# Kernel optimization log

Hardware: AMD Instinct MI355X
Metric: run time of the kernel (lower is better)

The kernel has to match this reference:

```python
import jax, jax.numpy as jnp
import numpy as np

N_NODES = 50000
N_EDGES = 800000
NIN = 128
NHID = 128
NLAYERS = 4
NOUT = 40
H = 0.1
EPS_BN = 1e-5
CG_ITERS = 10


def _bn(x, g, b, m, v):
    # eval-mode BatchNorm1d with running stats
    return (x - m) * jax.lax.rsqrt(v + EPS_BN) * g + b


def _forward(T, edge_index, Kopen_W, Kopen_b, bnO_g, bnO_b, bnO_m, bnO_v, conv_W, conv_b, bnA_g, bnA_b, bnA_m, bnA_v, Wq, bq, Wk, bk, mha_factor, KR1_W, KR1_b, KR2_W, KR2_b, KRU0_W, KRU0_b, bn_g, bn_b, bn_m, bn_v, Kappa, Kclose_W, Kclose_b):
    N = T.shape[0]
    L = KR1_W.shape[0]
    order = L
    row, col = edge_index[0], edge_index[1]
    # get_laplacian(sym) removes self-loops, so L = I - D^{-1/2} A D^{-1/2} on non-loop edges
    nonself = (row != col).astype(jnp.float32)
    deg = jax.ops.segment_sum(nonself, row, num_segments=N)
    dinv = jnp.where(deg > 0, jax.lax.rsqrt(jnp.maximum(deg, 1.0)), 0.0)
    lap_w = -(dinv[row] * dinv[col]) * nonself  # off-diagonal Laplacian weights; diagonal = 1

    Th = jax.nn.elu(_bn(T @ Kopen_W.T + Kopen_b, bnO_g, bnO_b, bnO_m, bnO_v))
    T0 = Th  # dropout is identity in eval mode
    # Conv1d(k=1) over `order` identical repeated history slots == one dense matmul
    z = jax.nn.relu(_bn(T0 @ conv_W.T + conv_b, bnA_g, bnA_b, bnA_m, bnA_v))
    acts = jnp.tile(z[None], (order, 1, 1))  # [order, N, nhid]
    nhid = Th.shape[1]
    scale = nhid ** -0.5  # single head -> head_dim = nhid
    rfac = jax.nn.relu(mha_factor[0])

    Tcur = Th
    for jj in range(L):
        # single-head self-attention weights over history axis (batch = nodes); output proj unused
        q = jnp.einsum('onh,dh->ond', acts, Wq) + bq
        k = jnp.einsum('onh,dh->ond', acts, Wk) + bk
        attn = jax.nn.softmax(jnp.einsum('ind,jnd->nij', q, k) * scale, axis=-1)  # [N, order, order]
        Cm = jnp.mean(jnp.log(attn * rfac + 1e-4), axis=0)
        Cm = 0.5 * (Cm + Cm.T)
        c = Cm[-1]
        c = c / jnp.sum(c)
        T1 = jnp.einsum('o,onh->nh', c, acts)
        # gated reaction MLP
        dT = T1 @ KR1_W[jj].T + KR1_b[jj] + T0 @ KRU0_W[jj].T + KRU0_b[jj]
        dT2 = T1 @ KR2_W[jj].T + KR2_b[jj]
        dT = dT + T1 * jnp.clip(dT2, -1.0, 1.0)
        Tr = jax.nn.elu(_bn(T1 + H * dT, bn_g[jj], bn_b[jj], bn_m[jj], bn_v[jj]))
        # implicit diffusion: CG iterations on (I + h*Kd*L) X = Tr
        Kd = jnp.clip(Kappa[jj], 0.0, 1.0)

        def matvec(Y):
            lapY = Y + jax.ops.segment_sum(lap_w[:, None] * Y[col], row, num_segments=N)
            return Y + H * (lapY * Kd)

        X, R, P = Tr, Tr, Tr
        normRold = jnp.sum(R * R)
        done = jnp.asarray(False)
        for _ in range(CG_ITERS):
            LP = matvec(P)
            alpha = jnp.sum(R * R) / (jnp.sum(P * LP) + 1e-6)
            Xn = X + alpha * P
            Rn = R - alpha * LP
            normR = jnp.sum(Rn * Rn)
            beta = normR / (normRold + 1e-6)
            Pn = Rn + beta * P
            X = jnp.where(done, X, Xn)
            R = jnp.where(done, R, Rn)
            done2 = done | (normR < 1e-5)  # early-break in torch -> freeze state
            P = jnp.where(done2, P, Pn)
            normRold = jnp.where(done2, normRold, normR)
            done = done2
        Tcur = X
        acts = jnp.concatenate([acts[1:], Tcur[None]], axis=0)
    return Tcur @ Kclose_W.T + Kclose_b


def setup_inputs():
    key = jax.random.key(0)
    ks = iter(jax.random.split(key, 64))
    f32 = jnp.float32

    def nrm(shape, s=0.05):
        return s * jax.random.normal(next(ks), shape, dtype=f32)

    def bn_params(shape):
        g = 1.0 + nrm(shape, 0.1)
        b = nrm(shape, 0.1)
        m = nrm(shape, 0.1)
        v = 1.0 + 0.1 * jax.random.uniform(next(ks), shape, dtype=f32)
        return g, b, m, v

    eye = jnp.eye(NHID, dtype=f32)
    d = {}
    d['T'] = jax.random.normal(next(ks), (N_NODES, NIN), dtype=f32)
    d['edge_index'] = jax.random.randint(next(ks), (2, N_EDGES), 0, N_NODES)
    d['Kopen_W'] = nrm((NHID, NIN), 0.08)
    d['Kopen_b'] = jnp.zeros((NHID,), f32)
    d['bnO_g'], d['bnO_b'], d['bnO_m'], d['bnO_v'] = bn_params((NHID,))
    d['conv_W'] = nrm((NHID, NHID), 0.08)
    d['conv_b'] = jnp.zeros((NHID,), f32)
    d['bnA_g'], d['bnA_b'], d['bnA_m'], d['bnA_v'] = bn_params((NHID,))
    d['Wq'] = nrm((NHID, NHID), 0.08)
    d['bq'] = jnp.zeros((NHID,), f32)
    d['Wk'] = nrm((NHID, NHID), 0.08)
    d['bk'] = jnp.zeros((NHID,), f32)
    d['mha_factor'] = jnp.array([10.0], dtype=f32)
    d['KR1_W'] = eye[None] + nrm((NLAYERS, NHID, NHID), 0.01)
    d['KR1_b'] = jnp.zeros((NLAYERS, NHID), f32)
    d['KR2_W'] = nrm((NLAYERS, NHID, NHID), 0.01)
    d['KR2_b'] = jnp.zeros((NLAYERS, NHID), f32)
    d['KRU0_W'] = eye[None] + nrm((NLAYERS, NHID, NHID), 0.01)
    d['KRU0_b'] = jnp.zeros((NLAYERS, NHID), f32)
    d['bn_g'], d['bn_b'], d['bn_m'], d['bn_v'] = bn_params((NLAYERS, NHID))
    d['Kappa'] = jax.random.uniform(next(ks), (NLAYERS, NHID), dtype=f32, minval=0.0, maxval=1.2)
    d['Kclose_W'] = nrm((NOUT, NHID), 0.08)
    d['Kclose_b'] = jnp.zeros((NOUT,), f32)
    return d


def reference(T, edge_index, Kopen_W, Kopen_b, bnO_g, bnO_b, bnO_m, bnO_v, conv_W, conv_b, bnA_g, bnA_b, bnA_m, bnA_v, Wq, bq, Wk, bk, mha_factor, KR1_W, KR1_b, KR2_W, KR2_b, KRU0_W, KRU0_b, bn_g, bn_b, bn_m, bn_v, Kappa, Kclose_W, Kclose_b):
    return _forward(T, edge_index, Kopen_W, Kopen_b, bnO_g, bnO_b, bnO_m, bnO_v, conv_W, conv_b, bnA_g, bnA_b, bnA_m, bnA_v, Wq, bq, Wk, bk, mha_factor, KR1_W, KR1_b, KR2_W, KR2_b, KRU0_W, KRU0_b, bn_g, bn_b, bn_m, bn_v, Kappa, Kclose_W, Kclose_b)
```

## Files before the change

kernel.cpp:

```cpp
#include <hip/hip_runtime.h>
#include <math.h>

#define N_NODES 50000
#define N_EDGES 800000
#define NHID    128
#define NOUT    40
#define NLAYERS 4
#define CG_ITERS 10
#define HSTEP   0.1f
#define EPS_BN  1e-5f

#define NB   (N_NODES * NHID)
#define NB4  (NB / 4)

#define EW_BLOCKS   2048
#define SPMV_BLOCKS 2048
#define ATTN_BLOCKS 1024
#define SCAN_BLOCKS 196

#define SLOT_RR   0
#define SLOT_PLP  10
#define SLOT_NR   20

__device__ __forceinline__ float wred64(float v) {
    v += __shfl_xor(v, 32, 64);
    v += __shfl_xor(v, 16, 64);
    v += __shfl_xor(v, 8, 64);
    v += __shfl_xor(v, 4, 64);
    v += __shfl_xor(v, 2, 64);
    v += __shfl_xor(v, 1, 64);
    return v;
}

__device__ __forceinline__ int wscan64(int v, int lane) {
    int incl = v;
    #pragma unroll
    for (int off = 1; off < 64; off <<= 1) {
        int t = __shfl_up(incl, off, 64);
        if (lane >= off) incl += t;
    }
    return incl;
}


__global__ void k_zero_i32(int* p, int n) {
    int i = blockIdx.x * blockDim.x + threadIdx.x;
    int stride = gridDim.x * blockDim.x;
    for (; i < n; i += stride) p[i] = 0;
}

__global__ void k_count(const int* __restrict__ row, const int* __restrict__ col, int* __restrict__ deg) {
    int e = blockIdx.x * 256 + threadIdx.x;
    if (e < N_EDGES) {
        int r = row[e], c = col[e];
        if (r != c) atomicAdd(&deg[r], 1);
    }
}

__global__ __launch_bounds__(256) void k_scan1(const int* __restrict__ deg,
                                               int* __restrict__ rowptr, int* __restrict__ blksum) {
    __shared__ int wsum[4];
    int tid = threadIdx.x, lane = tid & 63, wid = tid >> 6;
    int i = blockIdx.x * 256 + tid;
    int v = (i < N_NODES) ? deg[i] : 0;
    int incl = wscan64(v, lane);
    if (lane == 63) wsum[wid] = incl;
    __syncthreads();
    int wpre = 0;
    for (int w = 0; w < wid; w++) wpre += wsum[w];
    incl += wpre;
    if (i < N_NODES) rowptr[i + 1] = incl;
    if (tid == 255) blksum[blockIdx.x] = incl;
}

__global__ __launch_bounds__(256) void k_scan2(const int* __restrict__ blksum, int* __restrict__ blkoff) {
    __shared__ int wsum[4];
    int tid = threadIdx.x, lane = tid & 63, wid = tid >> 6;
    int v = (tid < SCAN_BLOCKS) ? blksum[tid] : 0;
    int incl = wscan64(v, lane);
    if (lane == 63) wsum[wid] = incl;
    __syncthreads();
    int wpre = 0;
    for (int w = 0; w < wid; w++) wpre += wsum[w];
    incl += wpre;
    if (tid < SCAN_BLOCKS) blkoff[tid] = incl - v;
}

__global__ __launch_bounds__(256) void k_scan3(const int* __restrict__ deg, const int* __restrict__ blkoff,
                                               int* __restrict__ rowptr, float* __restrict__ dinv,
                                               int* __restrict__ cursor) {
    int i = blockIdx.x * 256 + threadIdx.x;
    if (i == 0) rowptr[0] = 0;
    if (i < N_NODES) {
        int incl = rowptr[i + 1] + blkoff[blockIdx.x];
        rowptr[i + 1] = incl;
        int d = deg[i];
        cursor[i] = incl - d;
        dinv[i] = (d > 0) ? rsqrtf((float)d) : 0.0f;
    }
}

__global__ void k_scatter(const int* __restrict__ row, const int* __restrict__ col,
                          const float* __restrict__ dinv, int* __restrict__ cursor,
                          int* __restrict__ ecol, float* __restrict__ ew) {
    int e = blockIdx.x * 256 + threadIdx.x;
    if (e < N_EDGES) {
        int r = row[e], c = col[e];
        if (r != c) {
            int p = atomicAdd(&cursor[r], 1);
            ecol[p] = c;
            ew[p] = -dinv[r] * dinv[c];
        }
    }
}


__global__ void k_mmat(const float* __restrict__ Wq, const float* __restrict__ Wk, float* __restrict__ M) {
    int h1 = blockIdx.x, h2 = threadIdx.x;
    float s = 0.f;
    for (int d = 0; d < 128; ++d) s += Wq[d * 128 + h1] * Wk[d * 128 + h2];
    M[h1 * 128 + h2] = s;
}

__global__ void k_uv(const float* __restrict__ Wq, const float* __restrict__ Wk,
// ... 121 lines not shown
    int tid = threadIdx.x;
    int lane = tid & 63, wid = tid >> 6;
    const float* hp[4] = {h0, h1, h2, h3};
    const float* gp[4] = {g0, g1, g2, g3};
    float uu0 = u[lane], uu1 = u[lane + 64];
    float vv0 = v[lane], vv1 = v[lane + 64];
    float c0v = *c0p;
    float rf = mha[0]; rf = rf > 0.f ? rf : 0.f;
    const float scale = 0.08838834764831845f;

    float tacc = 0.f;
    int totalWaves = gridDim.x * 4;
    for (int n = blockIdx.x * 4 + wid; n < N_NODES; n += totalWaves) {
        float a0[4], a1[4], gg0[4], gg1[4];
        size_t base = (size_t)n * 128 + lane;
        #pragma unroll
        for (int o = 0; o < 4; o++) {
            a0[o] = hp[o][base];  a1[o] = hp[o][base + 64];
            gg0[o] = gp[o][base]; gg1[o] = gp[o][base + 64];
        }
        float s[4][4], pu[4], pv[4];
        #pragma unroll
        for (int i = 0; i < 4; i++) {
            pu[i] = wred64(uu0 * a0[i] + uu1 * a1[i]);
            pv[i] = wred64(vv0 * a0[i] + vv1 * a1[i]);
            #pragma unroll
            for (int j = 0; j < 4; j++)
                s[i][j] = wred64(a0[i] * gg0[j] + a1[i] * gg1[j]);
        }
        #pragma unroll
        for (int i = 0; i < 4; i++)
            #pragma unroll
            for (int j = 0; j < 4; j++)
                s[i][j] = scale * (s[i][j] + pu[j] + pv[i] + c0v);

        if (lane < 16) {
            int i = lane >> 2, j = lane & 3;
            float m = fmaxf(fmaxf(s[i][0], s[i][1]), fmaxf(s[i][2], s[i][3]));
            float den = expf(s[i][0] - m) + expf(s[i][1] - m) + expf(s[i][2] - m) + expf(s[i][3] - m);
            float attn = expf(s[i][j] - m) / den;
            tacc += logf(attn * rf + 1e-4f);
        }
    }
    __shared__ float accum[4][16];
    if (lane < 16) accum[wid][lane] = tacc;
    __syncthreads();
    if (tid < 16)
        atomicAdd(&Cm[tid], accum[0][tid] + accum[1][tid] + accum[2][tid] + accum[3][tid]);
}

__global__ void k_cvec(const float* __restrict__ Cm, float* __restrict__ c) {
    if (threadIdx.x == 0) {
        float cm[16];
        for (int i = 0; i < 16; i++) cm[i] = Cm[i] / (float)N_NODES;
        float cc[4];
        for (int j = 0; j < 4; j++) cc[j] = 0.5f * (cm[12 + j] + cm[j * 4 + 3]);
        float s = cc[0] + cc[1] + cc[2] + cc[3];
        for (int j = 0; j < 4; j++) c[j] = cc[j] / s;
    }
}

__global__ __launch_bounds__(256) void k_t1(
    const float* __restrict__ h0, const float* __restrict__ h1,
    const float* __restrict__ h2, const float* __restrict__ h3,
    const float* __restrict__ c, float* __restrict__ T1)
{
    float c0 = c[0], c1 = c[1], c2 = c[2], c3 = c[3];
    int stride = gridDim.x * blockDim.x;
    for (int i = blockIdx.x * blockDim.x + threadIdx.x; i < NB4; i += stride) {
        float4 x0 = ((const float4*)h0)[i];
        float4 x1 = ((const float4*)h1)[i];
        float4 x2 = ((const float4*)h2)[i];
        float4 x3 = ((const float4*)h3)[i];
        float4 o;
        o.x = c0 * x0.x + c1 * x1.x + c2 * x2.x + c3 * x3.x;
        o.y = c0 * x0.y + c1 * x1.y + c2 * x2.y + c3 * x3.y;
        o.z = c0 * x0.z + c1 * x1.z + c2 * x2.z + c3 * x3.z;
        o.w = c0 * x0.w + c1 * x1.w + c2 * x2.w + c3 * x3.w;
        ((float4*)T1)[i] = o;
    }
}


__global__ __launch_bounds__(256) void k_combine(
    const float* __restrict__ T1v, const float* __restrict__ M1v, const float* __restrict__ M2v,
    const float* __restrict__ g, const float* __restrict__ b,
    const float* __restrict__ m, const float* __restrict__ v,
    float* __restrict__ TRv)
{
    int stride = gridDim.x * blockDim.x;
    for (int i = blockIdx.x * blockDim.x + threadIdx.x; i < NB4; i += stride) {
        float4 t1 = ((const float4*)T1v)[i];
        float4 m1 = ((const float4*)M1v)[i];
        float4 m2 = ((const float4*)M2v)[i];
        int chb = (i * 4) & 127;
        float tt[4] = {t1.x, t1.y, t1.z, t1.w};
        float a1[4] = {m1.x, m1.y, m1.z, m1.w};
        float a2[4] = {m2.x, m2.y, m2.z, m2.w};
        float o[4];
        #pragma unroll
        for (int k = 0; k < 4; k++) {
            float cl = fminf(fmaxf(a2[k], -1.f), 1.f);
            float x = tt[k] + HSTEP * (a1[k] + tt[k] * cl);
            int ch = chb + k;
            float xb = (x - m[ch]) * rsqrtf(v[ch] + EPS_BN) * g[ch] + b[ch];
            o[k] = xb > 0.f ? xb : expm1f(xb);
        }
        ((float4*)TRv)[i] = make_float4(o[0], o[1], o[2], o[3]);
    }
}


__global__ __launch_bounds__(256) void k_cginit(const float* __restrict__ TR, float* __restrict__ X,
                                                float* __restrict__ R, float* __restrict__ scal, int* __restrict__ doneI) {
    if (blockIdx.x == 0) {
        if (threadIdx.x < 32) scal[threadIdx.x] = 0.f;
        if (threadIdx.x == 32) *doneI = 0;
    }
    int stride = gridDim.x * blockDim.x;
    for (int i = blockIdx.x * blockDim.x + threadIdx.x; i < NB4; i += stride) {
        float4 t = ((const float4*)TR)[i];
        ((float4*)X)[i] = t;
        ((float4*)R)[i] = t;
    }
}

__global__ __launch_bounds__(256) void k_spmv_lp(
    const int* __restrict__ rowptr, const int* __restrict__ ecol, const float* __restrict__ ew,
    const float* __restrict__ P, const float* __restrict__ R, const float* __restrict__ Kap,
    float* __restrict__ LP, float* __restrict__ scal, const int* __restrict__ doneI, int it)
{
    if (*doneI) return;
    int tid = threadIdx.x;
    int lane = tid & 63;
    int wid  = tid >> 6;
    float2 kd2 = ((const float2*)Kap)[lane];
    kd2.x = fminf(fmaxf(kd2.x, 0.f), 1.f);
    kd2.y = fminf(fmaxf(kd2.y, 0.f), 1.f);
    const float2* P2 = (const float2*)P;
    const float2* R2 = (const float2*)R;
    float2* LP2 = (float2*)LP;

    float pPLP = 0.f, pRR = 0.f;
    int totalWaves = gridDim.x * 4;
    for (int r = blockIdx.x * 4 + wid; r < N_NODES; r += totalWaves) {
        int e0 = rowptr[r], e1 = rowptr[r + 1];
        float ax = 0.f, ay = 0.f;
        int e = e0;
        for (; e + 4 <= e1; e += 4) {
            int c0 = ecol[e], c1 = ecol[e + 1], c2 = ecol[e + 2], c3 = ecol[e + 3];
            float w0 = ew[e], w1 = ew[e + 1], w2 = ew[e + 2], w3 = ew[e + 3];
            float2 p0 = P2[(size_t)c0 * 64 + lane];
            float2 p1 = P2[(size_t)c1 * 64 + lane];
            float2 p2 = P2[(size_t)c2 * 64 + lane];
            float2 p3 = P2[(size_t)c3 * 64 + lane];
            ax += w0 * p0.x + w1 * p1.x + w2 * p2.x + w3 * p3.x;
            ay += w0 * p0.y + w1 * p1.y + w2 * p2.y + w3 * p3.y;
        }
        for (; e < e1; ++e) {
            int c = ecol[e]; float w = ew[e];
            float2 p = P2[(size_t)c * 64 + lane];
            ax += w * p.x; ay += w * p.y;
        }
        size_t idx = (size_t)r * 64 + lane;
        float2 pv = P2[idx];
        float2 rv = R2[idx];
        float2 lp;
        lp.x = pv.x + HSTEP * (kd2.x * (pv.x + ax));
        lp.y = pv.y + HSTEP * (kd2.y * (pv.y + ay));
        LP2[idx] = lp;
        pPLP += pv.x * lp.x + pv.y * lp.y;
        pRR  += rv.x * rv.x + rv.y * rv.y;
    }
    pPLP = wred64(pPLP);
    pRR  = wred64(pRR);
    __shared__ float red[8];
    if (lane == 0) { red[wid] = pPLP; red[4 + wid] = pRR; }
    __syncthreads();
    if (tid == 0) {
        atomicAdd(&scal[SLOT_PLP + it], red[0] + red[1] + red[2] + red[3]);
        atomicAdd(&scal[SLOT_RR + it], red[4] + red[5] + red[6] + red[7]);
    }
}

__global__ __launch_bounds__(256) void k_xr(
    float* __restrict__ X, const float* __restrict__ P, const float* __restrict__ LP,
    float* __restrict__ R, float* __restrict__ scal, const int* __restrict__ doneI, int it)
{
    if (*doneI) return;
    float alpha = scal[SLOT_RR + it] / (scal[SLOT_PLP + it] + 1e-6f);
    float pNR = 0.f;
    int stride = gridDim.x * blockDim.x;
    for (int i = blockIdx.x * blockDim.x + threadIdx.x; i < NB4; i += stride) {
        float4 x = ((const float4*)X)[i];
        float4 p = ((const float4*)P)[i];
        float4 lp = ((const float4*)LP)[i];
        float4 r = ((const float4*)R)[i];
        x.x += alpha * p.x; x.y += alpha * p.y; x.z += alpha * p.z; x.w += alpha * p.w;
        r.x -= alpha * lp.x; r.y -= alpha * lp.y; r.z -= alpha * lp.z; r.w -= alpha * lp.w;
        ((float4*)X)[i] = x;
        ((float4*)R)[i] = r;
        pNR += r.x * r.x + r.y * r.y + r.z * r.z + r.w * r.w;
    }
    pNR = wred64(pNR);
    __shared__ float red[4];
    int lane = threadIdx.x & 63, wid = threadIdx.x >> 6;
    if (lane == 0) red[wid] = pNR;
    __syncthreads();
    if (threadIdx.x == 0)
        atomicAdd(&scal[SLOT_NR + it], red[0] + red[1] + red[2] + red[3]);
}

__global__ __launch_bounds__(256) void k_pupd(
    const float* __restrict__ R, float* __restrict__ P,
    const float* __restrict__ scal, int* __restrict__ doneI, int it)
{
    float nr = scal[SLOT_NR + it];
    int done2 = (*doneI) || (nr < 1e-5f);
    if (blockIdx.x == 0 && threadIdx.x == 0) *doneI = done2;
    if (done2) return;
    float nro = (it == 0) ? scal[SLOT_RR + 0] : scal[SLOT_NR + it - 1];
    float beta = nr / (nro + 1e-6f);
    int stride = gridDim.x * blockDim.x;
    for (int i = blockIdx.x * blockDim.x + threadIdx.x; i < NB4; i += stride) {
        float4 r = ((const float4*)R)[i];
        float4 p = ((const float4*)P)[i];
        p.x = r.x + beta * p.x; p.y = r.y + beta * p.y;
        p.z = r.z + beta * p.z; p.w = r.w + beta * p.w;
        ((float4*)P)[i] = p;
    }
}


extern "C" void kernel_launch(void* const* d_in, const int* in_sizes, int n_in,
                              void* d_out, int out_size, void* d_ws, size_t ws_size,
                              hipStream_t stream) {
    (void)in_sizes; (void)n_in; (void)out_size; (void)ws_size;

    const float* T      = (const float*)d_in[0];
    const int*   EI     = (const int*)d_in[1];
    const float* KopenW = (const float*)d_in[2];
    const float* Kopenb = (const float*)d_in[3];
    const float* bnOg   = (const float*)d_in[4];
    const float* bnOb   = (const float*)d_in[5];
    const float* bnOm   = (const float*)d_in[6];
    const float* bnOv   = (const float*)d_in[7];
    const float* convW  = (const float*)d_in[8];
    const float* convb  = (const float*)d_in[9];
    const float* bnAg   = (const float*)d_in[10];
    const float* bnAb   = (const float*)d_in[11];
    const float* bnAm   = (const float*)d_in[12];
    const float* bnAv   = (const float*)d_in[13];
    const float* Wq     = (const float*)d_in[14];
    const float* bq     = (const float*)d_in[15];
    const float* Wk     = (const float*)d_in[16];
    const float* bk     = (const float*)d_in[17];
    const float* mha    = (const float*)d_in[18];
    const float* KR1W   = (const float*)d_in[19];
    const float* KR1b   = (const float*)d_in[20];
    const float* KR2W   = (const float*)d_in[21];
    const float* KR2b   = (const float*)d_in[22];
    const float* KRU0W  = (const float*)d_in[23];
    const float* KRU0b  = (const float*)d_in[24];
    const float* bng    = (const float*)d_in[25];
    const float* bnbb   = (const float*)d_in[26];
    const float* bnm    = (const float*)d_in[27];
    const float* bnv    = (const float*)d_in[28];
    const float* Kappa  = (const float*)d_in[29];
    const float* KcloseW = (const float*)d_in[30];
    const float* Kcloseb = (const float*)d_in[31];

    const int* row = EI;
    const int* col = EI + N_EDGES;

    char* ws = (char*)d_ws;
    size_t off = 0;
    auto alloc = [&](size_t bytes) -> void* {
        void* p = ws + off;
        off += (bytes + 255) & ~(size_t)255;
        return p;
    };

    float* B[10];
    for (int i = 0; i < 10; i++) B[i] = (float*)alloc((size_t)NB * 4);
    int*   ecol   = (int*)alloc((size_t)N_EDGES * 4);
    float* ewt    = (float*)alloc((size_t)N_EDGES * 4);
    int*   rowptr = (int*)alloc((size_t)(N_NODES + 1) * 4);
    int*   cursor = (int*)alloc((size_t)N_NODES * 4);
    int*   deg    = (int*)alloc((size_t)N_NODES * 4);
    float* dinv   = (float*)alloc((size_t)N_NODES * 4);
    int*   blksum = (int*)alloc(256 * 4);
    int*   blkoff = (int*)alloc(256 * 4);
    float* Mmat   = (float*)alloc(128 * 128 * 4);
    float* uvec   = (float*)alloc(512);
    float* vvec   = (float*)alloc(512);
    float* c0s    = (float*)alloc(256);
    float* Cm     = (float*)alloc(256);
    float* cvec   = (float*)alloc(256);
    float* scal   = (float*)alloc(256);
    int*   doneI  = (int*)alloc(256);

    float* TH = B[0];
    float* Z  = B[1];
    float* XB[4] = {B[2], B[3], B[4], B[5]};
    float* G[4]  = {B[6], B[7], B[8], B[9]};
    float* M1 = G[0], *M2 = G[1], *TR = G[2], *T1 = G[3];
    float* LPb = G[1];
    float* Pb  = G[2];
    float* Rb  = G[3];

    k_zero_i32<<<196, 256, 0, stream>>>(deg, N_NODES);
    k_count<<<(N_EDGES + 255) / 256, 256, 0, stream>>>(row, col, deg);
    k_scan1<<<SCAN_BLOCKS, 256, 0, stream>>>(deg, rowptr, blksum);
    k_scan2<<<1, 256, 0, stream>>>(blksum, blkoff);
    k_scan3<<<SCAN_BLOCKS, 256, 0, stream>>>(deg, blkoff, rowptr, dinv, cursor);
    k_scatter<<<(N_EDGES + 255) / 256, 256, 0, stream>>>(row, col, dinv, cursor, ecol, ewt);

    k_mmat<<<128, 128, 0, stream>>>(Wq, Wk, Mmat);
    k_uv<<<1, 128, 0, stream>>>(Wq, Wk, bq, bk, uvec, vvec, c0s);

    const int GEMM_GRID = (N_NODES + 63) / 64;

    k_gemm128<<<GEMM_GRID, 256, 0, stream>>>(T, KopenW, Kopenb, TH, N_NODES, 1, 0, bnOg, bnOb, bnOm, bnOv);
    k_gemm128<<<GEMM_GRID, 256, 0, stream>>>(TH, convW, convb, Z, N_NODES, 2, 0, bnAg, bnAb, bnAm, bnAv);

    const float* hist[4] = {Z, Z, Z, Z};

    for (int jj = 0; jj < NLAYERS; jj++) {
        const float* uq[4];
        int nu = 0, gi[4];
        for (int i = 0; i < 4; i++) {
            int f = -1;
            for (int k = 0; k < nu; k++) if (uq[k] == hist[i]) f = k;
            if (f < 0) { uq[nu] = hist[i]; f = nu; nu++; }
            gi[i] = f;
        }
        for (int u = 0; u < nu; u++)
            k_gemm128<<<GEMM_GRID, 256, 0, stream>>>(uq[u], Mmat, nullptr, G[u], N_NODES, 0, 0,
                                                     nullptr, nullptr, nullptr, nullptr);
        k_zero16<<<1, 64, 0, stream>>>(Cm);
        k_attn<<<ATTN_BLOCKS, 256, 0, stream>>>(hist[0], hist[1], hist[2], hist[3],
                                                G[gi[0]], G[gi[1]], G[gi[2]], G[gi[3]],
                                                uvec, vvec, c0s, mha, Cm);
        k_cvec<<<1, 64, 0, stream>>>(Cm, cvec);
        k_t1<<<EW_BLOCKS, 256, 0, stream>>>(hist[0], hist[1], hist[2], hist[3], cvec, T1);

        k_gemm128<<<GEMM_GRID, 256, 0, stream>>>(T1, KR1W + (size_t)jj * 16384, KR1b + jj * 128, M1,
                                                 N_NODES, 0, 0, nullptr, nullptr, nullptr, nullptr);
        k_gemm128<<<GEMM_GRID, 256, 0, stream>>>(TH, KRU0W + (size_t)jj * 16384, KRU0b + jj * 128, M1,
                                                 N_NODES, 0, 1, nullptr, nullptr, nullptr, nullptr);
        k_gemm128<<<GEMM_GRID, 256, 0, stream>>>(T1, KR2W + (size_t)jj * 16384, KR2b + jj * 128, M2,
                                                 N_NODES, 0, 0, nullptr, nullptr, nullptr, nullptr);
        k_combine<<<EW_BLOCKS, 256, 0, stream>>>(T1, M1, M2,
                                                 bng + jj * 128, bnbb + jj * 128, bnm + jj * 128, bnv + jj * 128,
                                                 TR);

        k_cginit<<<EW_BLOCKS, 256, 0, stream>>>(TR, XB[jj], Rb, scal, doneI);
        for (int it = 0; it < CG_ITERS; it++) {
            k_spmv_lp<<<SPMV_BLOCKS, 256, 0, stream>>>(rowptr, ecol, ewt, Pb, Rb, Kappa + jj * 128,
                                                       LPb, scal, doneI, it);
            k_xr<<<EW_BLOCKS, 256, 0, stream>>>(XB[jj], Pb, LPb, Rb, scal, doneI, it);
            k_pupd<<<EW_BLOCKS, 256, 0, stream>>>(Rb, Pb, scal, doneI, it);
        }

        hist[0] = hist[1]; hist[1] = hist[2]; hist[2] = hist[3]; hist[3] = XB[jj];
    }

    k_close<<<(N_NODES + 255) / 256, 256, 0, stream>>>(XB[3], KcloseW, Kcloseb, (float*)d_out);
}
```

Baseline: 5.298 ms.

## Fuse CG updates and compute residual norm algebraically from SpMV dot products

The CG loop drops from three kernels per iteration to two. The SpMV kernel now also accumulates r·Ap and Ap·Ap, so the new residual norm comes from the expansion ||r - αAp||² and the x, r and p updates run in one pass. The initial copy kernel is folded into the BN/ELU combine kernel, which now writes P, X and R directly. The SpMV is also reorganised so each block handles one 16-channel slice for 16 rows at a time, and the attention grid size is doubled. The algebraic residual norm can lose precision through cancellation, and the channel-slice SpMV re-reads the edge lists once per slice.

```diff
diff --git a/kernel.cpp b/kernel.cpp
--- a/kernel.cpp
+++ b/kernel.cpp
@@ -15,12 +15,13 @@
 
 #define EW_BLOCKS   2048
 #define SPMV_BLOCKS 2048
-#define ATTN_BLOCKS 1024
+#define ATTN_BLOCKS 2048
 #define SCAN_BLOCKS 196
 
-#define SLOT_RR   0
-#define SLOT_PLP  10
-#define SLOT_NR   20
+#define SLOT_RR    0
+#define SLOT_PLP   10
+#define SLOT_RLP   20
+#define SLOT_LPLP  30
 
 __device__ __forceinline__ float wred64(float v) {
     v += __shfl_xor(v, 32, 64);
@@ -328,11 +329,16 @@
 
 
 __global__ __launch_bounds__(256) void k_combine(
-    const float* __restrict__ T1v, const float* __restrict__ M1v, const float* __restrict__ M2v,
+    const float* T1v, const float* __restrict__ M1v, const float* __restrict__ M2v,
     const float* __restrict__ g, const float* __restrict__ b,
     const float* __restrict__ m, const float* __restrict__ v,
-    float* __restrict__ TRv)
+    float* __restrict__ Pv, float* __restrict__ Xv, float* Rv,
+    float* __restrict__ scal, int* __restrict__ doneArr)
 {
+    if (blockIdx.x == 0) {
+        if (threadIdx.x < 40) scal[threadIdx.x] = 0.f;
+        if (threadIdx.x == 40) doneArr[0] = 0;
+    }
     int stride = gridDim.x * blockDim.x;
     for (int i = blockIdx.x * blockDim.x + threadIdx.x; i < NB4; i += stride) {
         float4 t1 = ((const float4*)T1v)[i];
@@ -351,90 +357,80 @@
             float xb = (x - m[ch]) * rsqrtf(v[ch] + EPS_BN) * g[ch] + b[ch];
             o[k] = xb > 0.f ? xb : expm1f(xb);
         }
-        ((float4*)TRv)[i] = make_float4(o[0], o[1], o[2], o[3]);
-    }
-}
-
-
-__global__ __launch_bounds__(256) void k_cginit(const float* __restrict__ TR, float* __restrict__ X,
-                                                float* __restrict__ R, float* __restrict__ scal, int* __restrict__ doneI) {
-    if (blockIdx.x == 0) {
-        if (threadIdx.x < 32) scal[threadIdx.x] = 0.f;
-        if (threadIdx.x == 32) *doneI = 0;
-    }
-    int stride = gridDim.x * blockDim.x;
-    for (int i = blockIdx.x * blockDim.x + threadIdx.x; i < NB4; i += stride) {
-        float4 t = ((const float4*)TR)[i];
-        ((float4*)X)[i] = t;
-        ((float4*)R)[i] = t;
-    }
-}
+        float4 o4 = make_float4(o[0], o[1], o[2], o[3]);
+        ((float4*)Pv)[i] = o4;
+        ((float4*)Xv)[i] = o4;
+        ((float4*)Rv)[i] = o4;
+    }
+}
+
 
 __global__ __launch_bounds__(256) void k_spmv_lp(
     const int* __restrict__ rowptr, const int* __restrict__ ecol, const float* __restrict__ ew,
     const float* __restrict__ P, const float* __restrict__ R, const float* __restrict__ Kap,
-    float* __restrict__ LP, float* __restrict__ scal, const int* __restrict__ doneI, int it)
+    float* __restrict__ LP, float* __restrict__ scal, const int* __restrict__ doneArr, int it)
 {
-    if (*doneI) return;
+    if (doneArr[it]) return;
     int tid = threadIdx.x;
-    int lane = tid & 63;
-    int wid  = tid >> 6;
-    float2 kd2 = ((const float2*)Kap)[lane];
-    kd2.x = fminf(fmaxf(kd2.x, 0.f), 1.f);
-    kd2.y = fminf(fmaxf(kd2.y, 0.f), 1.f);
-    const float2* P2 = (const float2*)P;
-    const float2* R2 = (const float2*)R;
-    float2* LP2 = (float2*)LP;
-
-    float pPLP = 0.f, pRR = 0.f;
-    int totalWaves = gridDim.x * 4;
-    for (int r = blockIdx.x * 4 + wid; r < N_NODES; r += totalWaves) {
+    int lane = tid & 63, wid = tid >> 6;
+    int q = lane >> 4;
+    int cl = lane & 15;
+    int slice = blockIdx.x & 7;
+    int sblk = blockIdx.x >> 3;
+    int ch = slice * 16 + cl;
+    float kd = fminf(fmaxf(Kap[ch], 0.f), 1.f);
+
+    float pPLP = 0.f, pRR = 0.f, pRLP = 0.f, pLPLP = 0.f;
+    const int rstride = (SPMV_BLOCKS / 8) * 16;
+    for (int r = sblk * 16 + wid * 4 + q; r < N_NODES; r += rstride) {
         int e0 = rowptr[r], e1 = rowptr[r + 1];
-        float ax = 0.f, ay = 0.f;
+        float acc = 0.f;
         int e = e0;
         for (; e + 4 <= e1; e += 4) {
             int c0 = ecol[e], c1 = ecol[e + 1], c2 = ecol[e + 2], c3 = ecol[e + 3];
             float w0 = ew[e], w1 = ew[e + 1], w2 = ew[e + 2], w3 = ew[e + 3];
-            float2 p0 = P2[(size_t)c0 * 64 + lane];
-            float2 p1 = P2[(size_t)c1 * 64 + lane];
-            float2 p2 = P2[(size_t)c2 * 64 + lane];
-            float2 p3 = P2[(size_t)c3 * 64 + lane];
-            ax += w0 * p0.x + w1 * p1.x + w2 * p2.x + w3 * p3.x;
-            ay += w0 * p0.y + w1 * p1.y + w2 * p2.y + w3 * p3.y;
-        }
-        for (; e < e1; ++e) {
-            int c = ecol[e]; float w = ew[e];
-            float2 p = P2[(size_t)c * 64 + lane];
-            ax += w * p.x; ay += w * p.y;
-        }
-        size_t idx = (size_t)r * 64 + lane;
-        float2 pv = P2[idx];
-        float2 rv = R2[idx];
-        float2 lp;
-        lp.x = pv.x + HSTEP * (kd2.x * (pv.x + ax));
-        lp.y = pv.y + HSTEP * (kd2.y * (pv.y + ay));
-        LP2[idx] = lp;
-        pPLP += pv.x * lp.x + pv.y * lp.y;
-        pRR  += rv.x * rv.x + rv.y * rv.y;
-    }
-    pPLP = wred64(pPLP);
-    pRR  = wred64(pRR);
-    __shared__ float red[8];
-    if (lane == 0) { red[wid] = pPLP; red[4 + wid] = pRR; }
+            acc += w0 * P[(size_t)c0 * 128 + ch] + w1 * P[(size_t)c1 * 128 + ch]
+                 + w2 * P[(size_t)c2 * 128 + ch] + w3 * P[(size_t)c3 * 128 + ch];
+        }
+        for (; e < e1; ++e)
+            acc += ew[e] * P[(size_t)ecol[e] * 128 + ch];
+        size_t idx = (size_t)r * 128 + ch;
+        float pv = P[idx];
+        float rv = R[idx];
+        float lp = pv + HSTEP * (kd * (pv + acc));
+        LP[idx] = lp;
+        pPLP  += pv * lp;
+        pRR   += rv * rv;
+        pRLP  += rv * lp;
+        pLPLP += lp * lp;
+    }
+    pPLP = wred64(pPLP); pRR = wred64(pRR); pRLP = wred64(pRLP); pLPLP = wred64(pLPLP);
+    __shared__ float red[16];
+    if (lane == 0) { red[wid] = pPLP; red[4 + wid] = pRR; red[8 + wid] = pRLP; red[12 + wid] = pLPLP; }
     __syncthreads();
     if (tid == 0) {
-        atomicAdd(&scal[SLOT_PLP + it], red[0] + red[1] + red[2] + red[3]);
-        atomicAdd(&scal[SLOT_RR + it], red[4] + red[5] + red[6] + red[7]);
-    }
-}
-
-__global__ __launch_bounds__(256) void k_xr(
-    float* __restrict__ X, const float* __restrict__ P, const float* __restrict__ LP,
-    float* __restrict__ R, float* __restrict__ scal, const int* __restrict__ doneI, int it)
+        atomicAdd(&scal[SLOT_PLP  + it], red[0] + red[1] + red[2] + red[3]);
+        atomicAdd(&scal[SLOT_RR   + it], red[4] + red[5] + red[6] + red[7]);
+        atomicAdd(&scal[SLOT_RLP  + it], red[8] + red[9] + red[10] + red[11]);
+        atomicAdd(&scal[SLOT_LPLP + it], red[12] + red[13] + red[14] + red[15]);
+    }
+}
+
+__global__ __launch_bounds__(256) void k_upd(
+    float* __restrict__ X, float* __restrict__ P, const float* __restrict__ LP,
+    float* __restrict__ R, const float* __restrict__ scal, int* __restrict__ doneArr, int it)
 {
-    if (*doneI) return;
-    float alpha = scal[SLOT_RR + it] / (scal[SLOT_PLP + it] + 1e-6f);
-    float pNR = 0.f;
+    int d = doneArr[it];
+    float RR   = scal[SLOT_RR + it];
+    float PLP  = scal[SLOT_PLP + it];
+    float RLP  = scal[SLOT_RLP + it];
+    float LPLP = scal[SLOT_LPLP + it];
+    float alpha = RR / (PLP + 1e-6f);
+    float nr = RR - 2.f * alpha * RLP + alpha * alpha * LPLP;
+    int d2 = d || (nr < 1e-5f);
+    if (blockIdx.x == 0 && threadIdx.x == 0) doneArr[it + 1] = d2;
+    if (d) return;
+    float beta = nr / (RR + 1e-6f);
     int stride = gridDim.x * blockDim.x;
     for (int i = blockIdx.x * blockDim.x + threadIdx.x; i < NB4; i += stride) {
         float4 x = ((const float4*)X)[i];
@@ -445,34 +441,11 @@
         r.x -= alpha * lp.x; r.y -= alpha * lp.y; r.z -= alpha * lp.z; r.w -= alpha * lp.w;
         ((float4*)X)[i] = x;
         ((float4*)R)[i] = r;
-        pNR += r.x * r.x + r.y * r.y + r.z * r.z + r.w * r.w;
-    }
-    pNR = wred64(pNR);
-    __shared__ float red[4];
-    int lane = threadIdx.x & 63, wid = threadIdx.x >> 6;
-    if (lane == 0) red[wid] = pNR;
-    __syncthreads();
-    if (threadIdx.x == 0)
-        atomicAdd(&scal[SLOT_NR + it], red[0] + red[1] + red[2] + red[3]);
-}
-
-__global__ __launch_bounds__(256) void k_pupd(
-    const float* __restrict__ R, float* __restrict__ P,
-    const float* __restrict__ scal, int* __restrict__ doneI, int it)
-{
-    float nr = scal[SLOT_NR + it];
-    int done2 = (*doneI) || (nr < 1e-5f);
-    if (blockIdx.x == 0 && threadIdx.x == 0) *doneI = done2;
-    if (done2) return;
-    float nro = (it == 0) ? scal[SLOT_RR + 0] : scal[SLOT_NR + it - 1];
-    float beta = nr / (nro + 1e-6f);
-    int stride = gridDim.x * blockDim.x;
-    for (int i = blockIdx.x * blockDim.x + threadIdx.x; i < NB4; i += stride) {
-        float4 r = ((const float4*)R)[i];
-        float4 p = ((const float4*)P)[i];
-        p.x = r.x + beta * p.x; p.y = r.y + beta * p.y;
-        p.z = r.z + beta * p.z; p.w = r.w + beta * p.w;
-        ((float4*)P)[i] = p;
+        if (!d2) {
+            p.x = r.x + beta * p.x; p.y = r.y + beta * p.y;
+            p.z = r.z + beta * p.z; p.w = r.w + beta * p.w;
+            ((float4*)P)[i] = p;
+        }
     }
 }
 
@@ -543,13 +516,13 @@
     float* Cm     = (float*)alloc(256);
     float* cvec   = (float*)alloc(256);
     float* scal   = (float*)alloc(256);
-    int*   doneI  = (int*)alloc(256);
+    int*   doneA  = (int*)alloc(256);
 
     float* TH = B[0];
     float* Z  = B[1];
     float* XB[4] = {B[2], B[3], B[4], B[5]};
     float* G[4]  = {B[6], B[7], B[8], B[9]};
-    float* M1 = G[0], *M2 = G[1], *TR = G[2], *T1 = G[3];
+    float* M1 = G[0], *M2 = G[1], *T1 = G[3];
     float* LPb = G[1];
     float* Pb  = G[2];
     float* Rb  = G[3];
@@ -598,14 +571,12 @@
                                                  N_NODES, 0, 0, nullptr, nullptr, nullptr, nullptr);
         k_combine<<<EW_BLOCKS, 256, 0, stream>>>(T1, M1, M2,
                                                  bng + jj * 128, bnbb + jj * 128, bnm + jj * 128, bnv + jj * 128,
-                                                 TR);
-
-        k_cginit<<<EW_BLOCKS, 256, 0, stream>>>(TR, XB[jj], Rb, scal, doneI);
+                                                 Pb, XB[jj], Rb, scal, doneA);
+
         for (int it = 0; it < CG_ITERS; it++) {
             k_spmv_lp<<<SPMV_BLOCKS, 256, 0, stream>>>(rowptr, ecol, ewt, Pb, Rb, Kappa + jj * 128,
-                                                       LPb, scal, doneI, it);
-            k_xr<<<EW_BLOCKS, 256, 0, stream>>>(XB[jj], Pb, LPb, Rb, scal, doneI, it);
-            k_pupd<<<EW_BLOCKS, 256, 0, stream>>>(Rb, Pb, scal, doneI, it);
+                                                       LPb, scal, doneA, it);
+            k_upd<<<EW_BLOCKS, 256, 0, stream>>>(XB[jj], Pb, LPb, Rb, scal, doneA, it);
         }
 
         hist[0] = hist[1]; hist[1] = hist[2]; hist[2] = hist[3]; hist[3] = XB[jj];
```

New measurement: 5.433 ms. 2.5% more time.

## Fuse combine and CG iterations into one cooperative persistent kernel

Applied to the files above, without the earlier changes.

Replaces the per-iteration launches (spmv, xr, pupd) and the combine/cginit kernels with a single cooperative kernel that uses grid-wide syncs between CG phases. Combine now writes P, X and R directly and computes the initial residual norm, which drops the separate init kernel and the redundant R·R pass inside spmv. Also widens the spmv unroll to 8 edges and doubles the attention grid. The cooperative grid is limited to resident blocks, and each grid.sync adds barrier latency in exchange for removing about 30 launches per layer.

```diff
diff --git a/kernel.cpp b/kernel.cpp
--- a/kernel.cpp
+++ b/kernel.cpp
@@ -1,5 +1,8 @@
 #include <hip/hip_runtime.h>
+#include <hip/hip_cooperative_groups.h>
 #include <math.h>
+
+namespace cgns = cooperative_groups;
 
 #define N_NODES 50000
 #define N_EDGES 800000
@@ -15,12 +18,12 @@
 
 #define EW_BLOCKS   2048
 #define SPMV_BLOCKS 2048
-#define ATTN_BLOCKS 1024
+#define ATTN_BLOCKS 2048
 #define SCAN_BLOCKS 196
 
-#define SLOT_RR   0
-#define SLOT_PLP  10
-#define SLOT_NR   20
+#define SLOT_RR0   0
+#define SLOT_PLP   1
+#define SLOT_NR    11
 
 __device__ __forceinline__ float wred64(float v) {
     v += __shfl_xor(v, 32, 64);
@@ -40,6 +43,115 @@
         if (lane >= off) incl += t;
     }
     return incl;
+}
+
+
+__device__ __forceinline__ float body_combine(
+    const float* T1v, const float* __restrict__ M1v, const float* M2v,
+    const float* __restrict__ bg, const float* __restrict__ bb,
+    const float* __restrict__ bm, const float* __restrict__ bv,
+    float* P, float* X, float* R, int gid, int gsize)
+{
+    float rr0 = 0.f;
+    for (int i = gid; i < NB4; i += gsize) {
+        float4 t1 = ((const float4*)T1v)[i];
+        float4 m1 = ((const float4*)M1v)[i];
+        float4 m2 = ((const float4*)M2v)[i];
+        int chb = (i * 4) & 127;
+        float tt[4] = {t1.x, t1.y, t1.z, t1.w};
+        float a1[4] = {m1.x, m1.y, m1.z, m1.w};
+        float a2[4] = {m2.x, m2.y, m2.z, m2.w};
+        float o[4];
+        #pragma unroll
+        for (int k = 0; k < 4; k++) {
+            float cl = fminf(fmaxf(a2[k], -1.f), 1.f);
+            float x = tt[k] + HSTEP * (a1[k] + tt[k] * cl);
+            int ch = chb + k;
+            float xb = (x - bm[ch]) * rsqrtf(bv[ch] + EPS_BN) * bg[ch] + bb[ch];
+            o[k] = xb > 0.f ? xb : expm1f(xb);
+            rr0 += o[k] * o[k];
+        }
+        float4 o4 = make_float4(o[0], o[1], o[2], o[3]);
+        ((float4*)P)[i] = o4;
+        ((float4*)X)[i] = o4;
+        ((float4*)R)[i] = o4;
+    }
+    return rr0;
+}
+
+__device__ __forceinline__ float body_spmv(
+    const int* __restrict__ rowptr, const int* __restrict__ ecol, const float* __restrict__ ewt,
+    const float2* __restrict__ P2, float2* __restrict__ LP2, float2 kd2,
+    int r0, int rstride, int lane)
+{
+    float pPLP = 0.f;
+    for (int r = r0; r < N_NODES; r += rstride) {
+        int e0 = rowptr[r], e1 = rowptr[r + 1];
+        float ax = 0.f, ay = 0.f;
+        int e = e0;
+        for (; e + 8 <= e1; e += 8) {
+            int   c0 = ecol[e],     c1 = ecol[e + 1], c2 = ecol[e + 2], c3 = ecol[e + 3];
+            int   c4 = ecol[e + 4], c5 = ecol[e + 5], c6 = ecol[e + 6], c7 = ecol[e + 7];
+            float w0 = ewt[e],     w1 = ewt[e + 1], w2 = ewt[e + 2], w3 = ewt[e + 3];
+            float w4 = ewt[e + 4], w5 = ewt[e + 5], w6 = ewt[e + 6], w7 = ewt[e + 7];
+            float2 p0 = P2[(size_t)c0 * 64 + lane];
+            float2 p1 = P2[(size_t)c1 * 64 + lane];
+            float2 p2 = P2[(size_t)c2 * 64 + lane];
+            float2 p3 = P2[(size_t)c3 * 64 + lane];
+            float2 p4 = P2[(size_t)c4 * 64 + lane];
+            float2 p5 = P2[(size_t)c5 * 64 + lane];
+            float2 p6 = P2[(size_t)c6 * 64 + lane];
+            float2 p7 = P2[(size_t)c7 * 64 + lane];
+            ax += w0 * p0.x + w1 * p1.x + w2 * p2.x + w3 * p3.x
+                + w4 * p4.x + w5 * p5.x + w6 * p6.x + w7 * p7.x;
+            ay += w0 * p0.y + w1 * p1.y + w2 * p2.y + w3 * p3.y
+                + w4 * p4.y + w5 * p5.y + w6 * p6.y + w7 * p7.y;
+        }
+        for (; e < e1; ++e) {
+            int c = ecol[e]; float w = ewt[e];
+            float2 p = P2[(size_t)c * 64 + lane];
+            ax += w * p.x; ay += w * p.y;
+        }
+        size_t idx = (size_t)r * 64 + lane;
+        float2 pv = P2[idx];
+        float2 lp;
+        lp.x = pv.x + HSTEP * (kd2.x * (pv.x + ax));
+        lp.y = pv.y + HSTEP * (kd2.y * (pv.y + ay));
+        LP2[idx] = lp;
+        pPLP += pv.x * lp.x + pv.y * lp.y;
+    }
+    return pPLP;
+}
+
+__device__ __forceinline__ float body_xr(
+    float* X, const float* __restrict__ P, const float* __restrict__ LP, float* R,
+    float alpha, int gid, int gsize)
+{
+    float pNR = 0.f;
+    for (int i = gid; i < NB4; i += gsize) {
+        float4 x = ((const float4*)X)[i];
+        float4 p = ((const float4*)P)[i];
+        float4 lp = ((const float4*)LP)[i];
+        float4 r = ((const float4*)R)[i];
+        x.x += alpha * p.x; x.y += alpha * p.y; x.z += alpha * p.z; x.w += alpha * p.w;
+        r.x -= alpha * lp.x; r.y -= alpha * lp.y; r.z -= alpha * lp.z; r.w -= alpha * lp.w;
+        ((float4*)X)[i] = x;
+        ((float4*)R)[i] = r;
+        pNR += r.x * r.x + r.y * r.y + r.z * r.z + r.w * r.w;
+    }
+    return pNR;
+}
+
+__device__ __forceinline__ void body_pupd(
+    const float* __restrict__ R, float* P, float beta, int gid, int gsize)
+{
+    for (int i = gid; i < NB4; i += gsize) {
+        float4 r = ((const float4*)R)[i];
+        float4 p = ((const float4*)P)[i];
+        p.x = r.x + beta * p.x; p.y = r.y + beta * p.y;
+        p.z = r.z + beta * p.z; p.w = r.w + beta * p.w;
+        ((float4*)P)[i] = p;
+    }
 }
 
 
@@ -327,153 +439,130 @@
 }
 
 
-__global__ __launch_bounds__(256) void k_combine(
-    const float* __restrict__ T1v, const float* __restrict__ M1v, const float* __restrict__ M2v,
-    const float* __restrict__ g, const float* __restrict__ b,
-    const float* __restrict__ m, const float* __restrict__ v,
-    float* __restrict__ TRv)
-{
-    int stride = gridDim.x * blockDim.x;
-    for (int i = blockIdx.x * blockDim.x + threadIdx.x; i < NB4; i += stride) {
-        float4 t1 = ((const float4*)T1v)[i];
-        float4 m1 = ((const float4*)M1v)[i];
-        float4 m2 = ((const float4*)M2v)[i];
-        int chb = (i * 4) & 127;
-        float tt[4] = {t1.x, t1.y, t1.z, t1.w};
-        float a1[4] = {m1.x, m1.y, m1.z, m1.w};
-        float a2[4] = {m2.x, m2.y, m2.z, m2.w};
-        float o[4];
-        #pragma unroll
-        for (int k = 0; k < 4; k++) {
-            float cl = fminf(fmaxf(a2[k], -1.f), 1.f);
-            float x = tt[k] + HSTEP * (a1[k] + tt[k] * cl);
-            int ch = chb + k;
-            float xb = (x - m[ch]) * rsqrtf(v[ch] + EPS_BN) * g[ch] + b[ch];
-            o[k] = xb > 0.f ? xb : expm1f(xb);
-        }
-        ((float4*)TRv)[i] = make_float4(o[0], o[1], o[2], o[3]);
-    }
-}
-
-
-__global__ __launch_bounds__(256) void k_cginit(const float* __restrict__ TR, float* __restrict__ X,
-                                                float* __restrict__ R, float* __restrict__ scal, int* __restrict__ doneI) {
-    if (blockIdx.x == 0) {
-        if (threadIdx.x < 32) scal[threadIdx.x] = 0.f;
-        if (threadIdx.x == 32) *doneI = 0;
-    }
-    int stride = gridDim.x * blockDim.x;
-    for (int i = blockIdx.x * blockDim.x + threadIdx.x; i < NB4; i += stride) {
-        float4 t = ((const float4*)TR)[i];
-        ((float4*)X)[i] = t;
-        ((float4*)R)[i] = t;
-    }
-}
-
-__global__ __launch_bounds__(256) void k_spmv_lp(
-    const int* __restrict__ rowptr, const int* __restrict__ ecol, const float* __restrict__ ew,
-    const float* __restrict__ P, const float* __restrict__ R, const float* __restrict__ Kap,
-    float* __restrict__ LP, float* __restrict__ scal, const int* __restrict__ doneI, int it)
-{
-    if (*doneI) return;
-    int tid = threadIdx.x;
-    int lane = tid & 63;
-    int wid  = tid >> 6;
+__global__ __launch_bounds__(256) void k_cg(
+    const float* T1v, const float* __restrict__ M1v, const float* M2v,
+    const float* __restrict__ bg, const float* __restrict__ bb,
+    const float* __restrict__ bm, const float* __restrict__ bv,
+    const float* __restrict__ Kap,
+    const int* __restrict__ rowptr, const int* __restrict__ ecol, const float* __restrict__ ewt,
+    float* P, float* X, float* R, float* LP,
+    float* scal)
+{
+    cgns::grid_group grid = cgns::this_grid();
+    int tid = threadIdx.x, lane = tid & 63, wid = tid >> 6;
+    int gid = blockIdx.x * 256 + tid;
+    int gsize = gridDim.x * 256;
+    __shared__ float red[8];
+
+    float rr0 = body_combine(T1v, M1v, M2v, bg, bb, bm, bv, P, X, R, gid, gsize);
+    rr0 = wred64(rr0);
+    if (lane == 0) red[wid] = rr0;
+    __syncthreads();
+    if (tid == 0) atomicAdd(&scal[SLOT_RR0], red[0] + red[1] + red[2] + red[3]);
+    grid.sync();
+
+    float RRcur = __hip_atomic_load(&scal[SLOT_RR0], __ATOMIC_RELAXED, __HIP_MEMORY_SCOPE_AGENT);
     float2 kd2 = ((const float2*)Kap)[lane];
     kd2.x = fminf(fmaxf(kd2.x, 0.f), 1.f);
     kd2.y = fminf(fmaxf(kd2.y, 0.f), 1.f);
-    const float2* P2 = (const float2*)P;
-    const float2* R2 = (const float2*)R;
-    float2* LP2 = (float2*)LP;
-
-    float pPLP = 0.f, pRR = 0.f;
     int totalWaves = gridDim.x * 4;
-    for (int r = blockIdx.x * 4 + wid; r < N_NODES; r += totalWaves) {
-        int e0 = rowptr[r], e1 = rowptr[r + 1];
-        float ax = 0.f, ay = 0.f;
-        int e = e0;
-        for (; e + 4 <= e1; e += 4) {
-            int c0 = ecol[e], c1 = ecol[e + 1], c2 = ecol[e + 2], c3 = ecol[e + 3];
-            float w0 = ew[e], w1 = ew[e + 1], w2 = ew[e + 2], w3 = ew[e + 3];
-            float2 p0 = P2[(size_t)c0 * 64 + lane];
-            float2 p1 = P2[(size_t)c1 * 64 + lane];
-            float2 p2 = P2[(size_t)c2 * 64 + lane];
-            float2 p3 = P2[(size_t)c3 * 64 + lane];
-            ax += w0 * p0.x + w1 * p1.x + w2 * p2.x + w3 * p3.x;
-            ay += w0 * p0.y + w1 * p1.y + w2 * p2.y + w3 * p3.y;
-        }
-        for (; e < e1; ++e) {
-            int c = ecol[e]; float w = ew[e];
-            float2 p = P2[(size_t)c * 64 + lane];
-            ax += w * p.x; ay += w * p.y;
-        }
-        size_t idx = (size_t)r * 64 + lane;
-        float2 pv = P2[idx];
-        float2 rv = R2[idx];
-        float2 lp;
-        lp.x = pv.x + HSTEP * (kd2.x * (pv.x + ax));
-        lp.y = pv.y + HSTEP * (kd2.y * (pv.y + ay));
-        LP2[idx] = lp;
-        pPLP += pv.x * lp.x + pv.y * lp.y;
-        pRR  += rv.x * rv.x + rv.y * rv.y;
-    }
+
+    for (int it = 0; it < CG_ITERS; ++it) {
+        float pPLP = body_spmv(rowptr, ecol, ewt, (const float2*)P, (float2*)LP, kd2,
+                               blockIdx.x * 4 + wid, totalWaves, lane);
+        pPLP = wred64(pPLP);
+        __syncthreads();
+        if (lane == 0) red[wid] = pPLP;
+        __syncthreads();
+        if (tid == 0) atomicAdd(&scal[SLOT_PLP + it], red[0] + red[1] + red[2] + red[3]);
+        grid.sync();
+
+        float PLP = __hip_atomic_load(&scal[SLOT_PLP + it], __ATOMIC_RELAXED, __HIP_MEMORY_SCOPE_AGENT);
+        float alpha = RRcur / (PLP + 1e-6f);
+        float pNR = body_xr(X, P, LP, R, alpha, gid, gsize);
+        pNR = wred64(pNR);
+        __syncthreads();
+        if (lane == 0) red[4 + wid] = pNR;
+        __syncthreads();
+        if (tid == 0) atomicAdd(&scal[SLOT_NR + it], red[4] + red[5] + red[6] + red[7]);
+        grid.sync();
+
+        float nr = __hip_atomic_load(&scal[SLOT_NR + it], __ATOMIC_RELAXED, __HIP_MEMORY_SCOPE_AGENT);
+        if (nr < 1e-5f) break;
+        float beta = nr / (RRcur + 1e-6f);
+        body_pupd(R, P, beta, gid, gsize);
+        RRcur = nr;
+        grid.sync();
+    }
+}
+
+
+__global__ __launch_bounds__(256) void f_combine(
+    const float* T1v, const float* __restrict__ M1v, const float* M2v,
+    const float* __restrict__ bg, const float* __restrict__ bb,
+    const float* __restrict__ bm, const float* __restrict__ bv,
+    float* P, float* X, float* R, float* scal, int* doneArr)
+{
+    int tid = threadIdx.x, lane = tid & 63, wid = tid >> 6;
+    if (blockIdx.x == 0 && tid == 0) doneArr[0] = 0;
+    int gid = blockIdx.x * 256 + tid;
+    int gsize = gridDim.x * 256;
+    float rr0 = body_combine(T1v, M1v, M2v, bg, bb, bm, bv, P, X, R, gid, gsize);
+    rr0 = wred64(rr0);
+    __shared__ float red[4];
+    if (lane == 0) red[wid] = rr0;
+    __syncthreads();
+    if (tid == 0) atomicAdd(&scal[SLOT_RR0], red[0] + red[1] + red[2] + red[3]);
+}
+
+__global__ __launch_bounds__(256) void f_spmv(
+    const int* __restrict__ rowptr, const int* __restrict__ ecol, const float* __restrict__ ewt,
+    const float* __restrict__ P, const float* __restrict__ Kap,
+    float* __restrict__ LP, float* __restrict__ scal, const int* __restrict__ doneArr, int it)
+{
+    if (doneArr[it]) return;
+    int tid = threadIdx.x, lane = tid & 63, wid = tid >> 6;
+    float2 kd2 = ((const float2*)Kap)[lane];
+    kd2.x = fminf(fmaxf(kd2.x, 0.f), 1.f);
+    kd2.y = fminf(fmaxf(kd2.y, 0.f), 1.f);
+    float pPLP = body_spmv(rowptr, ecol, ewt, (const float2*)P, (float2*)LP, kd2,
+                           blockIdx.x * 4 + wid, gridDim.x * 4, lane);
     pPLP = wred64(pPLP);
-    pRR  = wred64(pRR);
-    __shared__ float red[8];
-    if (lane == 0) { red[wid] = pPLP; red[4 + wid] = pRR; }
-    __syncthreads();
-    if (tid == 0) {
-        atomicAdd(&scal[SLOT_PLP + it], red[0] + red[1] + red[2] + red[3]);
-        atomicAdd(&scal[SLOT_RR + it], red[4] + red[5] + red[6] + red[7]);
-    }
-}
-
-__global__ __launch_bounds__(256) void k_xr(
-    float* __restrict__ X, const float* __restrict__ P, const float* __restrict__ LP,
-    float* __restrict__ R, float* __restrict__ scal, const int* __restrict__ doneI, int it)
-{
-    if (*doneI) return;
-    float alpha = scal[SLOT_RR + it] / (scal[SLOT_PLP + it] + 1e-6f);
-    float pNR = 0.f;
-    int stride = gridDim.x * blockDim.x;
-    for (int i = blockIdx.x * blockDim.x + threadIdx.x; i < NB4; i += stride) {
-        float4 x = ((const float4*)X)[i];
-        float4 p = ((const float4*)P)[i];
-        float4 lp = ((const float4*)LP)[i];
-        float4 r = ((const float4*)R)[i];
-        x.x += alpha * p.x; x.y += alpha * p.y; x.z += alpha * p.z; x.w += alpha * p.w;
-        r.x -= alpha * lp.x; r.y -= alpha * lp.y; r.z -= alpha * lp.z; r.w -= alpha * lp.w;
-        ((float4*)X)[i] = x;
-        ((float4*)R)[i] = r;
-        pNR += r.x * r.x + r.y * r.y + r.z * r.z + r.w * r.w;
-    }
+    __shared__ float red[4];
+    if (lane == 0) red[wid] = pPLP;
+    __syncthreads();
+    if (tid == 0) atomicAdd(&scal[SLOT_PLP + it], red[0] + red[1] + red[2] + red[3]);
+}
+
+__global__ __launch_bounds__(256) void f_xr(
+    float* X, const float* __restrict__ P, const float* __restrict__ LP, float* R,
+    float* __restrict__ scal, const int* __restrict__ doneArr, int it)
+{
+    if (doneArr[it]) return;
+    float RR = (it == 0) ? scal[SLOT_RR0] : scal[SLOT_NR + it - 1];
+    float alpha = RR / (scal[SLOT_PLP + it] + 1e-6f);
+    int gid = blockIdx.x * 256 + threadIdx.x;
+    float pNR = body_xr(X, P, LP, R, alpha, gid, gridDim.x * 256);
     pNR = wred64(pNR);
     __shared__ float red[4];
     int lane = threadIdx.x & 63, wid = threadIdx.x >> 6;
     if (lane == 0) red[wid] = pNR;
     __syncthreads();
-    if (threadIdx.x == 0)
-        atomicAdd(&scal[SLOT_NR + it], red[0] + red[1] + red[2] + red[3]);
-}
-
-__global__ __launch_bounds__(256) void k_pupd(
-    const float* __restrict__ R, float* __restrict__ P,
-    const float* __restrict__ scal, int* __restrict__ doneI, int it)
-{
+    if (threadIdx.x == 0) atomicAdd(&scal[SLOT_NR + it], red[0] + red[1] + red[2] + red[3]);
+}
+
+__global__ __launch_bounds__(256) void f_pupd(
+    const float* __restrict__ R, float* P,
+    const float* __restrict__ scal, int* doneArr, int it)
+{
+    if (doneArr[it]) { if (blockIdx.x == 0 && threadIdx.x == 0) doneArr[it + 1] = 1; return; }
     float nr = scal[SLOT_NR + it];
-    int done2 = (*doneI) || (nr < 1e-5f);
-    if (blockIdx.x == 0 && threadIdx.x == 0) *doneI = done2;
-    if (done2) return;
-    float nro = (it == 0) ? scal[SLOT_RR + 0] : scal[SLOT_NR + it - 1];
-    float beta = nr / (nro + 1e-6f);
-    int stride = gridDim.x * blockDim.x;
-    for (int i = blockIdx.x * blockDim.x + threadIdx.x; i < NB4; i += stride) {
-        float4 r = ((const float4*)R)[i];
-        float4 p = ((const float4*)P)[i];
-        p.x = r.x + beta * p.x; p.y = r.y + beta * p.y;
-        p.z = r.z + beta * p.z; p.w = r.w + beta * p.w;
-        ((float4*)P)[i] = p;
-    }
+    int d2 = (nr < 1e-5f);
+    if (blockIdx.x == 0 && threadIdx.x == 0) doneArr[it + 1] = d2;
+    if (d2) return;
+    float RR = (it == 0) ? scal[SLOT_RR0] : scal[SLOT_NR + it - 1];
+    float beta = nr / (RR + 1e-6f);
+    body_pupd(R, P, beta, blockIdx.x * 256 + threadIdx.x, gridDim.x * 256);
 }
 
 
@@ -543,16 +632,22 @@
     float* Cm     = (float*)alloc(256);
     float* cvec   = (float*)alloc(256);
     float* scal   = (float*)alloc(256);
-    int*   doneI  = (int*)alloc(256);
+    int*   doneA  = (int*)alloc(256);
 
     float* TH = B[0];
     float* Z  = B[1];
     float* XB[4] = {B[2], B[3], B[4], B[5]};
     float* G[4]  = {B[6], B[7], B[8], B[9]};
-    float* M1 = G[0], *M2 = G[1], *TR = G[2], *T1 = G[3];
+    float* M1 = G[0], *M2 = G[1], *T1 = G[3];
     float* LPb = G[1];
     float* Pb  = G[2];
     float* Rb  = G[3];
+
+    int occ = 0;
+    (void)hipOccupancyMaxActiveBlocksPerMultiprocessor(&occ, k_cg, 256, 0);
+    if (occ < 1) occ = 1;
+    int cgBlocks = occ * 256;
+    if (cgBlocks > 2048) cgBlocks = 2048;
 
     k_zero_i32<<<196, 256, 0, stream>>>(deg, N_NODES);
     k_count<<<(N_EDGES + 255) / 256, 256, 0, stream>>>(row, col, deg);
@@ -596,16 +691,33 @@
                                                  N_NODES, 0, 1, nullptr, nullptr, nullptr, nullptr);
         k_gemm128<<<GEMM_GRID, 256, 0, stream>>>(T1, KR2W + (size_t)jj * 16384, KR2b + jj * 128, M2,
                                                  N_NODES, 0, 0, nullptr, nullptr, nullptr, nullptr);
-        k_combine<<<EW_BLOCKS, 256, 0, stream>>>(T1, M1, M2,
-                                                 bng + jj * 128, bnbb + jj * 128, bnm + jj * 128, bnv + jj * 128,
-                                                 TR);
-
-        k_cginit<<<EW_BLOCKS, 256, 0, stream>>>(TR, XB[jj], Rb, scal, doneI);
-        for (int it = 0; it < CG_ITERS; it++) {
-            k_spmv_lp<<<SPMV_BLOCKS, 256, 0, stream>>>(rowptr, ecol, ewt, Pb, Rb, Kappa + jj * 128,
-                                                       LPb, scal, doneI, it);
-            k_xr<<<EW_BLOCKS, 256, 0, stream>>>(XB[jj], Pb, LPb, Rb, scal, doneI, it);
-            k_pupd<<<EW_BLOCKS, 256, 0, stream>>>(Rb, Pb, scal, doneI, it);
+
+        hipMemsetAsync(scal, 0, 128, stream);
+        const float* bgj  = bng  + jj * 128;
+        const float* bbj  = bnbb + jj * 128;
+        const float* bmj  = bnm  + jj * 128;
+        const float* bvj  = bnv  + jj * 128;
+        const float* kapj = Kappa + jj * 128;
+        float* Xj = XB[jj];
+        const float* T1c = T1; const float* M1c = M1; const float* M2c = M2;
+        void* cgArgs[] = {
+            (void*)&T1c, (void*)&M1c, (void*)&M2c,
+            (void*)&bgj, (void*)&bbj, (void*)&bmj, (void*)&bvj,
+            (void*)&kapj,
+            (void*)&rowptr, (void*)&ecol, (void*)&ewt,
+            (void*)&Pb, (void*)&Xj, (void*)&Rb, (void*)&LPb,
+            (void*)&scal
+        };
+        hipError_t ce = hipLaunchCooperativeKernel((const void*)k_cg, dim3(cgBlocks), dim3(256),
+                                                   cgArgs, 0, stream);
+        if (ce != hipSuccess) {
+            f_combine<<<EW_BLOCKS, 256, 0, stream>>>(T1c, M1c, M2c, bgj, bbj, bmj, bvj,
+                                                     Pb, Xj, Rb, scal, doneA);
+            for (int it = 0; it < CG_ITERS; it++) {
+                f_spmv<<<SPMV_BLOCKS, 256, 0, stream>>>(rowptr, ecol, ewt, Pb, kapj, LPb, scal, doneA, it);
+                f_xr<<<EW_BLOCKS, 256, 0, stream>>>(Xj, Pb, LPb, Rb, scal, doneA, it);
+                f_pupd<<<EW_BLOCKS, 256, 0, stream>>>(Rb, Pb, scal, doneA, it);
+            }
         }
 
         hist[0] = hist[1]; hist[1] = hist[2]; hist[2] = hist[3]; hist[3] = XB[jj];
```

After: 11.47 ms. 2.16x slower.
